# Performance work log

Hardware: AMD Instinct MI355X
Metric: run time of the kernel (lower is better)

Reference implementation:

```python
import jax, jax.numpy as jnp
import numpy as np

QUERY_DIM = 512
CAAN_DIM = 512
HID = 30

def setup_inputs() -> dict:
    key = jax.random.key(0)
    ks = jax.random.split(key, 9)
    def lin(kk, out_d, in_d):
        lim = 1.0 / np.sqrt(in_d)
        return jax.random.uniform(kk, (out_d, in_d), jnp.float32, -lim, lim)
    R = jax.random.normal(ks[0], (8, 2048, QUERY_DIM), jnp.float32)
    return {
        "R": R,
        "Wq": lin(ks[1], CAAN_DIM, QUERY_DIM), "bq": jnp.zeros((CAAN_DIM,), jnp.float32),
        "Wk": lin(ks[2], CAAN_DIM, QUERY_DIM), "bk": jnp.zeros((CAAN_DIM,), jnp.float32),
        "Wv": lin(ks[3], CAAN_DIM, QUERY_DIM), "bv": jnp.zeros((CAAN_DIM,), jnp.float32),
        "W1": lin(ks[4], HID, CAAN_DIM), "b1": jax.random.uniform(ks[5], (HID,), jnp.float32, -1/np.sqrt(CAAN_DIM), 1/np.sqrt(CAAN_DIM)),
        "W2": lin(ks[6], 1, HID), "b2": jax.random.uniform(ks[7], (1,), jnp.float32, -1/np.sqrt(HID), 1/np.sqrt(HID)),
    }

def reference(R, Wq, bq, Wk, bk, Wv, bv, W1, b1, W2, b2):
    # Projections: [b, n, d]
    Q = jnp.einsum('bnq,dq->bnd', R, Wq) + bq
    K = jnp.einsum('bnq,dq->bnd', R, Wk) + bk
    V = jnp.einsum('bnq,dq->bnd', R, Wv) + bv
    dk = K.shape[-1]
    # Full score matrix, naive exp-normalize (no max subtraction) as in original
    gamma = jnp.einsum('bnd,bmd->bnm', Q, K) / jnp.sqrt(jnp.float32(dk))
    e = jnp.exp(gamma)
    saat = e / jnp.sum(e, axis=2, keepdims=True)  # [b, n, n]
    a = jnp.einsum('bnm,bmd->bnd', saat, V)       # [b, n, d]
    # fc head: CAAN_dim -> 30 -> 1, squeeze last dim
    h = jnp.einsum('bnd,hd->bnh', a, W1) + b1
    winner_score = (jnp.einsum('bnh,oh->bno', h, W2) + b2)[..., 0]
    return winner_score
```

## Files before the change

kernel.cpp:

```cpp
#include <hip/hip_runtime.h>
#include <math.h>

#define BATCH 8
#define SEQ 2048
#define DIM 512
#define MTOT (BATCH*SEQ)
#define HID 30

typedef short bf16x8 __attribute__((ext_vector_type(8)));
typedef float f32x4 __attribute__((ext_vector_type(4)));

__device__ __forceinline__ unsigned short f2bf(float f) {
  unsigned int u = __float_as_uint(f);
  unsigned int r = (u + 0x7FFFu + ((u >> 16) & 1u)) >> 16;
  return (unsigned short)r;
}

__device__ __forceinline__ void gload_lds16(const void* g, void* l) {
  __builtin_amdgcn_global_load_lds((const __attribute__((address_space(1))) void*)g,
                                   (__attribute__((address_space(3))) void*)l, 16, 0, 0);
}

__device__ __forceinline__ void gemm256_core(const unsigned short* __restrict__ gA,
                                             const unsigned short* __restrict__ gB,
                                             char* smem, f32x4 (&acc)[8][4]) {
  const int t = threadIdx.x;
  const int lane = t & 63;
  const int w = t >> 6;
  const int wr = w >> 2, wc = w & 3;
  const int lr = lane & 15, kc = lane >> 4;
  const int ss = (t & 7) ^ ((t >> 3) & 7);
  const unsigned short* gsrc = (ss < 4 ? gA : gB) + (size_t)(t >> 3) * DIM + (ss & 3) * 8;
  const uint32_t dbase = (uint32_t)(t & 448) * 16;

  auto stage2 = [&](int slot, int kt, int qq) {
#pragma unroll
    for (int q = qq; q < qq + 2; ++q)
      gload_lds16(gsrc + (size_t)(q * 64) * DIM + kt * 32,
                  smem + slot * 32768 + q * 8192 + dbase);
  };

  stage2(0, 0, 0); stage2(0, 0, 2);
  stage2(1, 1, 0); stage2(1, 1, 2);
  asm volatile("s_waitcnt vmcnt(4)" ::: "memory");
  __builtin_amdgcn_s_barrier();
  asm volatile("" ::: "memory");

#pragma unroll
  for (int kt = 0; kt < 16; ++kt) {
    const char* Ab = smem + (kt % 3) * 32768;
    const int fslot = (kt + 2) % 3;
    const int src = (kt + 2 < 16) ? (kt + 2) : 15;
    bf16x8 bfr[4], af[4];
#pragma unroll
    for (int j = 0; j < 4; ++j) {
      int r = wc * 64 + j * 16 + lr;
      bfr[j] = *(const bf16x8*)(Ab + r * 128 + (((4 + kc) ^ (r & 7)) << 4));
    }
#pragma unroll
    for (int i = 0; i < 4; ++i) {
      int r = wr * 128 + i * 16 + lr;
      af[i] = *(const bf16x8*)(Ab + r * 128 + ((kc ^ (r & 7)) << 4));
    }
    __builtin_amdgcn_sched_barrier(0);
    stage2(fslot, src, 0);
    __builtin_amdgcn_s_barrier();
    asm volatile("s_waitcnt lgkmcnt(0)" ::: "memory");
    __builtin_amdgcn_sched_barrier(0);
    __builtin_amdgcn_s_setprio(1);
#pragma unroll
    for (int i = 0; i < 4; ++i)
#pragma unroll
      for (int j = 0; j < 4; ++j)
        acc[i][j] = __builtin_amdgcn_mfma_f32_16x16x32_bf16(af[i], bfr[j], acc[i][j], 0, 0, 0);
    __builtin_amdgcn_s_setprio(0);
    __builtin_amdgcn_sched_barrier(0);
    __builtin_amdgcn_s_barrier();
#pragma unroll
    for (int i = 0; i < 4; ++i) {
      int r = wr * 128 + (i + 4) * 16 + lr;
      af[i] = *(const bf16x8*)(Ab + r * 128 + ((kc ^ (r & 7)) << 4));
    }
    __builtin_amdgcn_sched_barrier(0);
    stage2(fslot, src, 2);
    __builtin_amdgcn_s_barrier();
    asm volatile("s_waitcnt lgkmcnt(0)" ::: "memory");
    __builtin_amdgcn_sched_barrier(0);
    __builtin_amdgcn_s_setprio(1);
#pragma unroll
    for (int i = 0; i < 4; ++i)
#pragma unroll
      for (int j = 0; j < 4; ++j)
        acc[i + 4][j] = __builtin_amdgcn_mfma_f32_16x16x32_bf16(af[i], bfr[j], acc[i + 4][j], 0, 0, 0);
    __builtin_amdgcn_s_setprio(0);
    __builtin_amdgcn_sched_barrier(0);
    asm volatile("s_waitcnt vmcnt(4)" ::: "memory");
    __builtin_amdgcn_s_barrier();
    asm volatile("" ::: "memory");
  }
}

__global__ __launch_bounds__(256) void k_weights(
    const float* __restrict__ Wq, const float* __restrict__ Wk, const float* __restrict__ Wv,
    const float* __restrict__ bq, const float* __restrict__ bv,
    const float* __restrict__ W1, const float* __restrict__ b1,
    const float* __restrict__ W2, const float* __restrict__ b2,
    unsigned short* __restrict__ Gt, float* __restrict__ u,
    float* __restrict__ wv2, float* __restrict__ consts) {
  __shared__ __align__(16) float As[16][68];
  __shared__ __align__(16) float Bs[16][68];
  __shared__ float vecs[512];
  __shared__ float red2[16][17];
  const int bid = blockIdx.x;
  const int t = threadIdx.x;

  if (bid < 64) {
    int tm = t & 15, tn = t >> 4;
    int q1b = (bid & 7) * 64, q2b = (bid >> 3) * 64;
    int lk = t >> 4, lc = (t & 15) * 4;
    float acc[4][4] = {};
    float4 ra = *(const float4*)&Wq[(size_t)lk * DIM + q1b + lc];
    float4 rb = *(const float4*)&Wk[(size_t)lk * DIM + q2b + lc];
    for (int kb = 0; kb < DIM; kb += 16) {
      *(float4*)&As[lk][lc] = ra;
      *(float4*)&Bs[lk][lc] = rb;
      __syncthreads();
      if (kb + 16 < DIM) {
        ra = *(const float4*)&Wq[(size_t)(kb + 16 + lk) * DIM + q1b + lc];
        rb = *(const float4*)&Wk[(size_t)(kb + 16 + lk) * DIM + q2b + lc];
      }
#pragma unroll
      for (int k = 0; k < 16; ++k) {
        float4 av = *(float4*)&As[k][tm * 4];
        float4 bv4 = *(float4*)&Bs[k][tn * 4];
        float a[4] = {av.x, av.y, av.z, av.w};
        float b[4] = {bv4.x, bv4.y, bv4.z, bv4.w};
#pragma unroll
        for (int i = 0; i < 4; ++i)
#pragma unroll
          for (int j = 0; j < 4; ++j) acc[i][j] = fmaf(a[i], b[j], acc[i][j]);
      }
      __syncthreads();
    }
#pragma unroll
    for (int i = 0; i < 4; ++i)
#pragma unroll
      for (int j = 0; j < 4; ++j)
        Gt[(size_t)(q2b + tn * 4 + j) * DIM + (q1b + tm * 4 + i)] = f2bf(acc[i][j]);
    return;
  }

  if (bid < 128) {
    bool isU = bid < 96;
    int qb = (bid - (isU ? 64 : 96)) * 16;
    if (isU) {
      vecs[t] = bq[t];
      vecs[t + 256] = bq[t + 256];
    } else {
      for (int d = t; d < DIM; d += 256) {
        float s = 0.f;
        for (int j = 0; j < HID; ++j) s = fmaf(W2[j], W1[(size_t)j * DIM + d], s);
        vecs[d] = s;
      }
    }
    __syncthreads();
    const float* M = isU ? Wk : Wv;
    int ql = t & 15, ds = t >> 4;
    float s = 0.f;
#pragma unroll 8
    for (int i = 0; i < 32; ++i) {
      int d = ds * 32 + i;
      s = fmaf(vecs[d], M[(size_t)d * DIM + qb + ql], s);
    }
    red2[ds][ql] = s;
    __syncthreads();
    if (t < 16) {
      float r = 0.f;
#pragma unroll
      for (int k = 0; k < 16; ++k) r += red2[k][t];
      (isU ? u : wv2)[qb + t] = r;
    }
    return;
  }

  {
    for (int d = t; d < DIM; d += 256) {
      float s = 0.f;
      for (int j = 0; j < HID; ++j) s = fmaf(W2[j], W1[(size_t)j * DIM + d], s);
      vecs[d] = s;
    }
    __syncthreads();
    float* red = (float*)red2;
    red[t] = bv[t] * vecs[t] + bv[t + 256] * vecs[t + 256];
    __syncthreads();
    for (int o = 128; o > 0; o >>= 1) {
      if (t < o) red[t] += red[t + o];
      __syncthreads();
    }
    if (t == 0) {
      consts[0] = red[0];
      float s = b2[0];
      for (int j = 0; j < HID; ++j) s = fmaf(W2[j], b1[j], s);
      consts[1] = s;
    }
  }
}

__global__ __launch_bounds__(256) void k_conv(const float* __restrict__ R,
                                              const float* __restrict__ wv2,
                                              const float* __restrict__ consts,
                                              unsigned short* __restrict__ Rb16,
                                              float* __restrict__ vw) {
  int wave = threadIdx.x >> 6, lane = threadIdx.x & 63;
  size_t n = (size_t)blockIdx.x * 4 + wave;
  const float* p = &R[n * DIM + lane * 8];
  float4 r0 = *(const float4*)p;
  float4 r1 = *(const float4*)(p + 4);
  ushort4 lo, hi;
  lo.x = f2bf(r0.x); lo.y = f2bf(r0.y); lo.z = f2bf(r0.z); lo.w = f2bf(r0.w);
  hi.x = f2bf(r1.x); hi.y = f2bf(r1.y); hi.z = f2bf(r1.z); hi.w = f2bf(r1.w);
  *(ushort4*)&Rb16[n * DIM + lane * 8] = lo;
  *(ushort4*)&Rb16[n * DIM + lane * 8 + 4] = hi;
  float4 v0 = *(const float4*)&wv2[lane * 8];
  float4 v1 = *(const float4*)&wv2[lane * 8 + 4];
  float sv = r0.x * v0.x + r0.y * v0.y + r0.z * v0.z + r0.w * v0.w +
             r1.x * v1.x + r1.y * v1.y + r1.z * v1.z + r1.w * v1.w;
#pragma unroll
  for (int o = 32; o > 0; o >>= 1) sv += __shfl_xor(sv, o);
  if (lane == 0) vw[n] = sv + consts[0];
}

__global__ __launch_bounds__(512, 2) void k_projT(const unsigned short* __restrict__ Rb16,
                                                  const unsigned short* __restrict__ Gt,
                                                  const float* __restrict__ u,
                                                  unsigned short* __restrict__ Tb16) {
  __shared__ __align__(16) char smem[98304];
  __shared__ float u_lds[256];
  int t = threadIdx.x;
  size_t rowb = (size_t)blockIdx.x * 256;
  int colb = blockIdx.y * 256;
  if (t < 256) u_lds[t] = u[colb + t];
  f32x4 acc[8][4] = {};
  gemm256_core(Rb16 + rowb * DIM, Gt + (size_t)colb * DIM, smem, acc);
  int lane = t & 63, w = t >> 6, wr = w >> 2, wc = w & 3;
  int lr = lane & 15, kq = lane >> 4;
#pragma unroll
  for (int i = 0; i < 8; ++i)
#pragma unroll
    for (int j = 0; j < 4; ++j)
#pragma unroll
      for (int r = 0; r < 4; ++r) {
        int row = wr * 128 + i * 16 + kq * 4 + r;
        int col = wc * 64 + j * 16 + lr;
        Tb16[(rowb + row) * DIM + colb + col] = f2bf(acc[i][j][r] + u_lds[col]);
      }
}

__global__ __launch_bounds__(512, 2) void k_qk(const unsigned short* __restrict__ Tb16,
                                               const unsigned short* __restrict__ Rb16,
                                               const float* __restrict__ vw,
                                               float* __restrict__ part_s1,
                                               float* __restrict__ part_den) {
  __shared__ __align__(16) char smem[98304];
  __shared__ float vw_lds[256];
  __shared__ float red_s1[4][256], red_den[4][256];
  int t = threadIdx.x;
  int orig = blockIdx.x;
  int wgid = (orig & 7) * 64 + (orig >> 3);
  int b = wgid >> 6;
  int nb = ((wgid >> 3) & 7) * 256;
  int mb = (wgid & 7) * 256;
  if (t < 256) vw_lds[t] = vw[b * SEQ + mb + t];
  f32x4 acc[8][4] = {};
  gemm256_core(Tb16 + ((size_t)b * SEQ + nb) * DIM,
               Rb16 + ((size_t)b * SEQ + mb) * DIM, smem, acc);
  int lane = t & 63, w = t >> 6, wr = w >> 2, wc = w & 3;
  int lr = lane & 15, kq = lane >> 4;
  const float rs = 0.044194173824159216f;
  float vwl[4];
#pragma unroll
  for (int j = 0; j < 4; ++j) vwl[j] = vw_lds[wc * 64 + j * 16 + lr];
#pragma unroll
  for (int i = 0; i < 8; ++i) {
#pragma unroll
    for (int r = 0; r < 4; ++r) {
      float sa = 0.f, sd = 0.f;
#pragma unroll
      for (int j = 0; j < 4; ++j) {
        float e = __expf(acc[i][j][r] * rs);
        sa = fmaf(e, vwl[j], sa);
        sd += e;
      }
#pragma unroll
      for (int m = 1; m < 16; m <<= 1) { sa += __shfl_xor(sa, m); sd += __shfl_xor(sd, m); }
      if (lr == 0) {
        int rl = wr * 128 + i * 16 + kq * 4 + r;
        red_s1[wc][rl] = sa;
        red_den[wc][rl] = sd;
      }
    }
  }
  __syncthreads();
  if (t < 256) {
    size_t o = ((size_t)b * 8 + (mb >> 8)) * SEQ + nb + t;
    part_s1[o] = red_s1[0][t] + red_s1[1][t] + red_s1[2][t] + red_s1[3][t];
    part_den[o] = red_den[0][t] + red_den[1][t] + red_den[2][t] + red_den[3][t];
  }
}

__global__ void k_final(const float* __restrict__ part_s1, const float* __restrict__ part_den,
                        const float* __restrict__ consts, float* __restrict__ out) {
  int n = blockIdx.x * 256 + threadIdx.x;
  int b = n >> 11, nn = n & 2047;
  float s1 = 0.f, dn = 0.f;
#pragma unroll
  for (int i = 0; i < 8; ++i) {
    size_t o = ((size_t)b * 8 + i) * SEQ + nn;
    s1 += part_s1[o];
    dn += part_den[o];
  }
  out[n] = s1 / dn + consts[1];
}

extern "C" void kernel_launch(void* const* d_in, const int* in_sizes, int n_in,
                              void* d_out, int out_size, void* d_ws, size_t ws_size,
                              hipStream_t stream) {
  const float* R  = (const float*)d_in[0];
  const float* Wq = (const float*)d_in[1];
  const float* bq = (const float*)d_in[2];
  const float* Wk = (const float*)d_in[3];
  const float* bk = (const float*)d_in[4];
  const float* Wv = (const float*)d_in[5];
  const float* bv = (const float*)d_in[6];
  const float* W1 = (const float*)d_in[7];
  const float* b1 = (const float*)d_in[8];
  const float* W2 = (const float*)d_in[9];
  const float* b2 = (const float*)d_in[10];
  (void)bk;
  float* out = (float*)d_out;

  char* p = (char*)d_ws;
  unsigned short* Rb16 = (unsigned short*)p; p += (size_t)MTOT * DIM * 2;
  unsigned short* Tb16 = (unsigned short*)p; p += (size_t)MTOT * DIM * 2;
  unsigned short* Gt   = (unsigned short*)p; p += (size_t)DIM * DIM * 2;
  float* part_s1  = (float*)p; p += (size_t)BATCH * 8 * SEQ * 4;
  float* part_den = (float*)p; p += (size_t)BATCH * 8 * SEQ * 4;
  float* u      = (float*)p; p += DIM * 4;
  float* wv2    = (float*)p; p += DIM * 4;
  float* vw     = (float*)p; p += MTOT * 4;
  float* consts = (float*)p; p += 16;

  hipLaunchKernelGGL(k_weights, dim3(129), dim3(256), 0, stream,
                     Wq, Wk, Wv, bq, bv, W1, b1, W2, b2, Gt, u, wv2, consts);
  hipLaunchKernelGGL(k_conv, dim3(MTOT / 4), dim3(256), 0, stream, R, wv2, consts, Rb16, vw);
  hipLaunchKernelGGL(k_projT, dim3(MTOT / 256, DIM / 256), dim3(512), 0, stream,
                     Rb16, Gt, u, Tb16);
  hipLaunchKernelGGL(k_qk, dim3(512), dim3(512), 0, stream, Tb16, Rb16, vw, part_s1, part_den);
  hipLaunchKernelGGL(k_final, dim3(MTOT / 256), dim3(256), 0, stream,
                     part_s1, part_den, consts, out);
}
```

Baseline: 98.29 us.

## Merge weight prep with R conversion, shrink projT tiles, fuse vw computation

Merges the weight-precompute and R-to-bf16 conversion into a single launch. The Gt tiles become 32x32 so more blocks run at once, and the vw row-dot with wv2 moves into the y==0 column blocks of the projection GEMM, reading Rb16. The projection GEMM drops from 256x256 tiles with 512 threads to 128x128 tiles with 256 threads for more blocks. The 256 GEMM core now loads both A halves up front and drops the mid-iteration barriers. consts[0] is added in k_final instead of into vw. The aims are one fewer launch, less serialized prep work and better occupancy; the risks are lower per-block data reuse and vw now computed from bf16-rounded R.

```diff
diff --git a/kernel.cpp b/kernel.cpp
--- a/kernel.cpp
+++ b/kernel.cpp
@@ -14,6 +14,9 @@
   unsigned int u = __float_as_uint(f);
   unsigned int r = (u + 0x7FFFu + ((u >> 16) & 1u)) >> 16;
   return (unsigned short)r;
+}
+__device__ __forceinline__ float bf2f(unsigned short u) {
+  return __uint_as_float((unsigned int)u << 16);
 }
 
 __device__ __forceinline__ void gload_lds16(const void* g, void* l) {
@@ -33,15 +36,14 @@
   const unsigned short* gsrc = (ss < 4 ? gA : gB) + (size_t)(t >> 3) * DIM + (ss & 3) * 8;
   const uint32_t dbase = (uint32_t)(t & 448) * 16;
 
-  auto stage2 = [&](int slot, int kt, int qq) {
-#pragma unroll
-    for (int q = qq; q < qq + 2; ++q)
+  auto stage = [&](int slot, int kt) {
+#pragma unroll
+    for (int q = 0; q < 4; ++q)
       gload_lds16(gsrc + (size_t)(q * 64) * DIM + kt * 32,
                   smem + slot * 32768 + q * 8192 + dbase);
   };
 
-  stage2(0, 0, 0); stage2(0, 0, 2);
-  stage2(1, 1, 0); stage2(1, 1, 2);
+  stage(0, 0); stage(1, 1);
   asm volatile("s_waitcnt vmcnt(4)" ::: "memory");
   __builtin_amdgcn_s_barrier();
   asm volatile("" ::: "memory");
@@ -51,7 +53,7 @@
     const char* Ab = smem + (kt % 3) * 32768;
     const int fslot = (kt + 2) % 3;
     const int src = (kt + 2 < 16) ? (kt + 2) : 15;
-    bf16x8 bfr[4], af[4];
+    bf16x8 bfr[4], af[4], af2[4];
 #pragma unroll
     for (int j = 0; j < 4; ++j) {
       int r = wc * 64 + j * 16 + lr;
@@ -63,9 +65,13 @@
       af[i] = *(const bf16x8*)(Ab + r * 128 + ((kc ^ (r & 7)) << 4));
     }
     __builtin_amdgcn_sched_barrier(0);
-    stage2(fslot, src, 0);
-    __builtin_amdgcn_s_barrier();
-    asm volatile("s_waitcnt lgkmcnt(0)" ::: "memory");
+#pragma unroll
+    for (int i = 0; i < 4; ++i) {
+      int r = wr * 128 + (i + 4) * 16 + lr;
+      af2[i] = *(const bf16x8*)(Ab + r * 128 + ((kc ^ (r & 7)) << 4));
+    }
+    __builtin_amdgcn_sched_barrier(0);
+    stage(fslot, src);
     __builtin_amdgcn_sched_barrier(0);
     __builtin_amdgcn_s_setprio(1);
 #pragma unroll
@@ -75,23 +81,12 @@
         acc[i][j] = __builtin_amdgcn_mfma_f32_16x16x32_bf16(af[i], bfr[j], acc[i][j], 0, 0, 0);
     __builtin_amdgcn_s_setprio(0);
     __builtin_amdgcn_sched_barrier(0);
-    __builtin_amdgcn_s_barrier();
-#pragma unroll
-    for (int i = 0; i < 4; ++i) {
-      int r = wr * 128 + (i + 4) * 16 + lr;
-      af[i] = *(const bf16x8*)(Ab + r * 128 + ((kc ^ (r & 7)) << 4));
-    }
-    __builtin_amdgcn_sched_barrier(0);
-    stage2(fslot, src, 2);
-    __builtin_amdgcn_s_barrier();
-    asm volatile("s_waitcnt lgkmcnt(0)" ::: "memory");
-    __builtin_amdgcn_sched_barrier(0);
     __builtin_amdgcn_s_setprio(1);
 #pragma unroll
     for (int i = 0; i < 4; ++i)
 #pragma unroll
       for (int j = 0; j < 4; ++j)
-        acc[i + 4][j] = __builtin_amdgcn_mfma_f32_16x16x32_bf16(af[i], bfr[j], acc[i + 4][j], 0, 0, 0);
+        acc[i + 4][j] = __builtin_amdgcn_mfma_f32_16x16x32_bf16(af2[i], bfr[j], acc[i + 4][j], 0, 0, 0);
     __builtin_amdgcn_s_setprio(0);
     __builtin_amdgcn_sched_barrier(0);
     asm volatile("s_waitcnt vmcnt(4)" ::: "memory");
@@ -100,59 +95,116 @@
   }
 }
 
-__global__ __launch_bounds__(256) void k_weights(
-    const float* __restrict__ Wq, const float* __restrict__ Wk, const float* __restrict__ Wv,
-    const float* __restrict__ bq, const float* __restrict__ bv,
+__device__ __forceinline__ void gemm128_core(const unsigned short* __restrict__ gA,
+                                             const unsigned short* __restrict__ gB,
+                                             char* smem, f32x4 (&acc)[4][4]) {
+  const int t = threadIdx.x;
+  const int lane = t & 63;
+  const int w = t >> 6;
+  const int wr = w >> 1, wc = w & 1;
+  const int lr = lane & 15, kc = lane >> 4;
+  const int ss = (t & 7) ^ ((t >> 3) & 7);
+  const unsigned short* gsrc = (ss < 4 ? gA : gB) + (size_t)(t >> 3) * DIM + (ss & 3) * 8;
+  const uint32_t dbase = (uint32_t)(t & 192) * 16;
+
+  auto stage = [&](int slot, int kt) {
+#pragma unroll
+    for (int q = 0; q < 4; ++q)
+      gload_lds16(gsrc + (size_t)(q * 32) * DIM + kt * 32,
+                  smem + slot * 16384 + q * 4096 + dbase);
+  };
+
+  stage(0, 0); stage(1, 1);
+  asm volatile("s_waitcnt vmcnt(4)" ::: "memory");
+  __builtin_amdgcn_s_barrier();
+  asm volatile("" ::: "memory");
+
+#pragma unroll
+  for (int kt = 0; kt < 16; ++kt) {
+    const char* Ab = smem + (kt % 3) * 16384;
+    const int fslot = (kt + 2) % 3;
+    const int src = (kt + 2 < 16) ? (kt + 2) : 15;
+    bf16x8 bfr[4], af[4];
+#pragma unroll
+    for (int j = 0; j < 4; ++j) {
+      int r = wc * 64 + j * 16 + lr;
+      bfr[j] = *(const bf16x8*)(Ab + r * 128 + (((4 + kc) ^ (r & 7)) << 4));
+    }
+#pragma unroll
+    for (int i = 0; i < 4; ++i) {
+      int r = wr * 64 + i * 16 + lr;
+      af[i] = *(const bf16x8*)(Ab + r * 128 + ((kc ^ (r & 7)) << 4));
+    }
+    __builtin_amdgcn_sched_barrier(0);
+    stage(fslot, src);
+    __builtin_amdgcn_sched_barrier(0);
+    __builtin_amdgcn_s_setprio(1);
+#pragma unroll
+    for (int i = 0; i < 4; ++i)
+#pragma unroll
+      for (int j = 0; j < 4; ++j)
+        acc[i][j] = __builtin_amdgcn_mfma_f32_16x16x32_bf16(af[i], bfr[j], acc[i][j], 0, 0, 0);
+    __builtin_amdgcn_s_setprio(0);
+    __builtin_amdgcn_sched_barrier(0);
+    asm volatile("s_waitcnt vmcnt(4)" ::: "memory");
+    __builtin_amdgcn_s_barrier();
+    asm volatile("" ::: "memory");
+  }
+}
+
+__global__ __launch_bounds__(256) void k_prep(
+    const float* __restrict__ R, const float* __restrict__ Wq, const float* __restrict__ Wk,
+    const float* __restrict__ Wv, const float* __restrict__ bq, const float* __restrict__ bv,
     const float* __restrict__ W1, const float* __restrict__ b1,
     const float* __restrict__ W2, const float* __restrict__ b2,
-    unsigned short* __restrict__ Gt, float* __restrict__ u,
-    float* __restrict__ wv2, float* __restrict__ consts) {
-  __shared__ __align__(16) float As[16][68];
-  __shared__ __align__(16) float Bs[16][68];
+    unsigned short* __restrict__ Gt, unsigned short* __restrict__ Rb16,
+    float* __restrict__ u, float* __restrict__ wv2, float* __restrict__ consts) {
+  __shared__ __align__(16) float As[16][34];
+  __shared__ __align__(16) float Bs[16][34];
   __shared__ float vecs[512];
   __shared__ float red2[16][17];
   const int bid = blockIdx.x;
   const int t = threadIdx.x;
 
-  if (bid < 64) {
+  if (bid >= 321) {
+    size_t base = ((size_t)(bid - 321) * 256 + t) * 8;
+    float4 r0 = *(const float4*)&R[base];
+    float4 r1 = *(const float4*)&R[base + 4];
+    ushort4 lo, hi;
+    lo.x = f2bf(r0.x); lo.y = f2bf(r0.y); lo.z = f2bf(r0.z); lo.w = f2bf(r0.w);
+    hi.x = f2bf(r1.x); hi.y = f2bf(r1.y); hi.z = f2bf(r1.z); hi.w = f2bf(r1.w);
+    *(ushort4*)&Rb16[base] = lo;
+    *(ushort4*)&Rb16[base + 4] = hi;
+    return;
+  }
+  if (bid < 256) {
     int tm = t & 15, tn = t >> 4;
-    int q1b = (bid & 7) * 64, q2b = (bid >> 3) * 64;
-    int lk = t >> 4, lc = (t & 15) * 4;
-    float acc[4][4] = {};
-    float4 ra = *(const float4*)&Wq[(size_t)lk * DIM + q1b + lc];
-    float4 rb = *(const float4*)&Wk[(size_t)lk * DIM + q2b + lc];
+    int q1b = (bid & 15) * 32, q2b = (bid >> 4) * 32;
+    int lk = t >> 4, lc = (t & 15) * 2;
+    float acc[2][2] = {};
     for (int kb = 0; kb < DIM; kb += 16) {
-      *(float4*)&As[lk][lc] = ra;
-      *(float4*)&Bs[lk][lc] = rb;
+      *(float2*)&As[lk][lc] = *(const float2*)&Wq[(size_t)(kb + lk) * DIM + q1b + lc];
+      *(float2*)&Bs[lk][lc] = *(const float2*)&Wk[(size_t)(kb + lk) * DIM + q2b + lc];
       __syncthreads();
-      if (kb + 16 < DIM) {
-        ra = *(const float4*)&Wq[(size_t)(kb + 16 + lk) * DIM + q1b + lc];
-        rb = *(const float4*)&Wk[(size_t)(kb + 16 + lk) * DIM + q2b + lc];
-      }
 #pragma unroll
       for (int k = 0; k < 16; ++k) {
-        float4 av = *(float4*)&As[k][tm * 4];
-        float4 bv4 = *(float4*)&Bs[k][tn * 4];
-        float a[4] = {av.x, av.y, av.z, av.w};
-        float b[4] = {bv4.x, bv4.y, bv4.z, bv4.w};
-#pragma unroll
-        for (int i = 0; i < 4; ++i)
-#pragma unroll
-          for (int j = 0; j < 4; ++j) acc[i][j] = fmaf(a[i], b[j], acc[i][j]);
+        float a0 = As[k][tm * 2], a1 = As[k][tm * 2 + 1];
+        float b0 = Bs[k][tn * 2], b1v = Bs[k][tn * 2 + 1];
+        acc[0][0] = fmaf(a0, b0, acc[0][0]); acc[0][1] = fmaf(a0, b1v, acc[0][1]);
+        acc[1][0] = fmaf(a1, b0, acc[1][0]); acc[1][1] = fmaf(a1, b1v, acc[1][1]);
       }
       __syncthreads();
     }
 #pragma unroll
-    for (int i = 0; i < 4; ++i)
-#pragma unroll
-      for (int j = 0; j < 4; ++j)
-        Gt[(size_t)(q2b + tn * 4 + j) * DIM + (q1b + tm * 4 + i)] = f2bf(acc[i][j]);
+    for (int i = 0; i < 2; ++i)
+#pragma unroll
+      for (int j = 0; j < 2; ++j)
+        Gt[(size_t)(q2b + tn * 2 + j) * DIM + (q1b + tm * 2 + i)] = f2bf(acc[i][j]);
     return;
   }
-
-  if (bid < 128) {
-    bool isU = bid < 96;
-    int qb = (bid - (isU ? 64 : 96)) * 16;
+  if (bid < 320) {
+    bool isU = bid < 288;
+    int qb = (bid - (isU ? 256 : 288)) * 16;
     if (isU) {
       vecs[t] = bq[t];
       vecs[t + 256] = bq[t + 256];
@@ -182,7 +234,6 @@
     }
     return;
   }
-
   {
     for (int d = t; d < DIM; d += 256) {
       float s = 0.f;
@@ -206,54 +257,50 @@
   }
 }
 
-__global__ __launch_bounds__(256) void k_conv(const float* __restrict__ R,
-                                              const float* __restrict__ wv2,
-                                              const float* __restrict__ consts,
-                                              unsigned short* __restrict__ Rb16,
-                                              float* __restrict__ vw) {
-  int wave = threadIdx.x >> 6, lane = threadIdx.x & 63;
-  size_t n = (size_t)blockIdx.x * 4 + wave;
-  const float* p = &R[n * DIM + lane * 8];
-  float4 r0 = *(const float4*)p;
-  float4 r1 = *(const float4*)(p + 4);
-  ushort4 lo, hi;
-  lo.x = f2bf(r0.x); lo.y = f2bf(r0.y); lo.z = f2bf(r0.z); lo.w = f2bf(r0.w);
-  hi.x = f2bf(r1.x); hi.y = f2bf(r1.y); hi.z = f2bf(r1.z); hi.w = f2bf(r1.w);
-  *(ushort4*)&Rb16[n * DIM + lane * 8] = lo;
-  *(ushort4*)&Rb16[n * DIM + lane * 8 + 4] = hi;
-  float4 v0 = *(const float4*)&wv2[lane * 8];
-  float4 v1 = *(const float4*)&wv2[lane * 8 + 4];
-  float sv = r0.x * v0.x + r0.y * v0.y + r0.z * v0.z + r0.w * v0.w +
-             r1.x * v1.x + r1.y * v1.y + r1.z * v1.z + r1.w * v1.w;
-#pragma unroll
-  for (int o = 32; o > 0; o >>= 1) sv += __shfl_xor(sv, o);
-  if (lane == 0) vw[n] = sv + consts[0];
-}
-
-__global__ __launch_bounds__(512, 2) void k_projT(const unsigned short* __restrict__ Rb16,
+__global__ __launch_bounds__(256, 2) void k_projT(const unsigned short* __restrict__ Rb16,
                                                   const unsigned short* __restrict__ Gt,
                                                   const float* __restrict__ u,
-                                                  unsigned short* __restrict__ Tb16) {
-  __shared__ __align__(16) char smem[98304];
-  __shared__ float u_lds[256];
+                                                  const float* __restrict__ wv2,
+                                                  unsigned short* __restrict__ Tb16,
+                                                  float* __restrict__ vw) {
+  __shared__ __align__(16) char smem[49152];
+  __shared__ float u_lds[128];
   int t = threadIdx.x;
-  size_t rowb = (size_t)blockIdx.x * 256;
-  int colb = blockIdx.y * 256;
-  if (t < 256) u_lds[t] = u[colb + t];
-  f32x4 acc[8][4] = {};
-  gemm256_core(Rb16 + rowb * DIM, Gt + (size_t)colb * DIM, smem, acc);
-  int lane = t & 63, w = t >> 6, wr = w >> 2, wc = w & 3;
+  size_t rowb = (size_t)blockIdx.x * 128;
+  int colb = blockIdx.y * 128;
+  if (t < 128) u_lds[t] = u[colb + t];
+  f32x4 acc[4][4] = {};
+  gemm128_core(Rb16 + rowb * DIM, Gt + (size_t)colb * DIM, smem, acc);
+  int lane = t & 63, w = t >> 6, wr = w >> 1, wc = w & 1;
   int lr = lane & 15, kq = lane >> 4;
 #pragma unroll
-  for (int i = 0; i < 8; ++i)
+  for (int i = 0; i < 4; ++i)
 #pragma unroll
     for (int j = 0; j < 4; ++j)
 #pragma unroll
       for (int r = 0; r < 4; ++r) {
-        int row = wr * 128 + i * 16 + kq * 4 + r;
+        int row = wr * 64 + i * 16 + kq * 4 + r;
         int col = wc * 64 + j * 16 + lr;
         Tb16[(rowb + row) * DIM + colb + col] = f2bf(acc[i][j][r] + u_lds[col]);
       }
+  if (blockIdx.y == 0) {
+    float* wv2s = (float*)smem;
+    __syncthreads();
+    if (t < 256) { wv2s[t] = wv2[t]; wv2s[t + 256] = wv2[t + 256]; }
+    __syncthreads();
+    int row = (int)rowb + (t >> 1);
+    const unsigned short* rp = Rb16 + (size_t)row * DIM + (t & 1) * 256;
+    const float* wp = wv2s + (t & 1) * 256;
+    float s = 0.f;
+#pragma unroll 8
+    for (int i = 0; i < 32; ++i) {
+      bf16x8 v = *(const bf16x8*)(rp + i * 8);
+#pragma unroll
+      for (int e = 0; e < 8; ++e) s = fmaf(bf2f((unsigned short)v[e]), wp[i * 8 + e], s);
+    }
+    s += __shfl_xor(s, 1);
+    if ((t & 1) == 0) vw[row] = s;
+  }
 }
 
 __global__ __launch_bounds__(512, 2) void k_qk(const unsigned short* __restrict__ Tb16,
@@ -319,7 +366,7 @@
     s1 += part_s1[o];
     dn += part_den[o];
   }
-  out[n] = s1 / dn + consts[1];
+  out[n] = s1 / dn + consts[0] + consts[1];
 }
 
 extern "C" void kernel_launch(void* const* d_in, const int* in_sizes, int n_in,
@@ -350,11 +397,10 @@
   float* vw     = (float*)p; p += MTOT * 4;
   float* consts = (float*)p; p += 16;
 
-  hipLaunchKernelGGL(k_weights, dim3(129), dim3(256), 0, stream,
-                     Wq, Wk, Wv, bq, bv, W1, b1, W2, b2, Gt, u, wv2, consts);
-  hipLaunchKernelGGL(k_conv, dim3(MTOT / 4), dim3(256), 0, stream, R, wv2, consts, Rb16, vw);
-  hipLaunchKernelGGL(k_projT, dim3(MTOT / 256, DIM / 256), dim3(512), 0, stream,
-                     Rb16, Gt, u, Tb16);
+  hipLaunchKernelGGL(k_prep, dim3(321 + MTOT * DIM / (256 * 8)), dim3(256), 0, stream,
+                     R, Wq, Wk, Wv, bq, bv, W1, b1, W2, b2, Gt, Rb16, u, wv2, consts);
+  hipLaunchKernelGGL(k_projT, dim3(MTOT / 128, DIM / 128), dim3(256), 0, stream,
+                     Rb16, Gt, u, wv2, Tb16, vw);
   hipLaunchKernelGGL(k_qk, dim3(512), dim3(512), 0, stream, Tb16, Rb16, vw, part_s1, part_den);
   hipLaunchKernelGGL(k_final, dim3(MTOT / 256), dim3(256), 0, stream,
                      part_s1, part_den, consts, out);
```

Result: faster. 95.87 us (-2.5%).
